# Kernel optimization log

Hardware: AMD Instinct MI355X
Metric: run time of the kernel (lower is better)

The kernel has to match this reference:

```python
import jax, jax.numpy as jnp
import numpy as np

N = 100_000      # nodes
E = 1_600_000    # edges (avg degree 16)
D = 64           # input_dim == hidden_dim
C = 10           # output classes
G = 512          # graphs in batch
L = 5            # num_layers (L-1 = 4 GINConv layers)
BN_EPS = 1e-5


def setup_inputs() -> dict:
    key = jax.random.key(0)
    ks = jax.random.split(key, 16)
    x = jax.random.normal(ks[0], (N, D), dtype=jnp.float32)
    edge_index = jax.random.randint(ks[1], (2, E), 0, N, dtype=jnp.int32)
    batch = jnp.sort(jax.random.randint(ks[2], (N,), 0, G, dtype=jnp.int32))
    s = 1.0 / np.sqrt(D)
    Lc = L - 1
    return {
        "x": x,
        "edge_index": edge_index,
        "batch": batch,
        "eps": jnp.zeros((Lc,), jnp.float32),                                   # GINConv eps (train_eps, init 0)
        "W1": jax.random.uniform(ks[3], (Lc, D, D), jnp.float32, -s, s),        # MLP linear 1
        "b1": jax.random.uniform(ks[4], (Lc, D), jnp.float32, -s, s),
        "g1": jnp.ones((Lc, D), jnp.float32),                                   # MLP BatchNorm
        "be1": jnp.zeros((Lc, D), jnp.float32),
        "W2": jax.random.uniform(ks[5], (Lc, D, D), jnp.float32, -s, s),        # MLP linear 2
        "b2": jax.random.uniform(ks[6], (Lc, D), jnp.float32, -s, s),
        "gout": jnp.ones((Lc, D), jnp.float32),                                 # outer BatchNorm
        "beout": jnp.zeros((Lc, D), jnp.float32),
        "Wp": jax.random.uniform(ks[7], (L, D, C), jnp.float32, -s, s),         # prediction linears
        "bp": jax.random.uniform(ks[8], (L, C), jnp.float32, -s, s),
    }


def _batchnorm(h, gamma, beta):
    # training-mode BN over node dim, biased variance (torch semantics)
    m = jnp.mean(h, axis=0)
    v = jnp.mean(jnp.square(h - m), axis=0)
    return gamma * (h - m) * jax.lax.rsqrt(v + BN_EPS) + beta


def reference(x, edge_index, batch, eps, W1, b1, g1, be1, W2, b2, gout, beout, Wp, bp):
    src, dst = edge_index[0], edge_index[1]
    hidden_rep = [x]
    h = x
    for l in range(L - 1):
        # GINConv: (1 + eps) * x + scatter-add of neighbor features
        agg = jax.ops.segment_sum(h[src], dst, num_segments=N)
        z = (1.0 + eps[l]) * h + agg
        # 2-layer MLP with internal BN+ReLU
        z = z @ W1[l] + b1[l]
        z = jax.nn.relu(_batchnorm(z, g1[l], be1[l]))
        z = z @ W2[l] + b2[l]
        # outer BN + ReLU
        h = jax.nn.relu(_batchnorm(z, gout[l], beout[l]))
        hidden_rep.append(h)
    # jumping-knowledge readout: per-layer global_add_pool + linear (dropout off / eval)
    score = jnp.zeros((G, C), jnp.float32)
    for l, hl in enumerate(hidden_rep):
        pooled = jax.ops.segment_sum(hl, batch, num_segments=G)
        score = score + pooled @ Wp[l] + bp[l]
    return score
```

## Files before the change

### kernel.cpp

```cpp
#include <hip/hip_runtime.h>

#define NN 100000
#define EE 1600000
#define DD 64
#define CC 10
#define GG 512
#define LL 5
#define NPAD 100352
#define N64 (NN * DD)
#define NB 392
#define PCH 4096
#define BCAP 6144
#define SC 8
#define PREPG 1563

typedef short bf16x8 __attribute__((ext_vector_type(8)));
typedef float f32x4  __attribute__((ext_vector_type(4)));
union U16 { uint4 u; bf16x8 h; };

__device__ __forceinline__ float bits2f(unsigned int b) { return __uint_as_float(b); }
__device__ __forceinline__ float bf2f(unsigned short s) { return __uint_as_float((unsigned int)s << 16); }
__device__ __forceinline__ unsigned short f2bf_rne(float v) {
    unsigned int b = __float_as_uint(v);
    return (unsigned short)((b + 0x7fffu + ((b >> 16) & 1u)) >> 16);
}
__device__ __forceinline__ void unpack8(uint4 u, float* f) {
    f[0] = bits2f(u.x << 16); f[1] = bits2f(u.x & 0xffff0000u);
    f[2] = bits2f(u.y << 16); f[3] = bits2f(u.y & 0xffff0000u);
    f[4] = bits2f(u.z << 16); f[5] = bits2f(u.z & 0xffff0000u);
    f[6] = bits2f(u.w << 16); f[7] = bits2f(u.w & 0xffff0000u);
}
__device__ __forceinline__ uint4 pack8(const float* f) {
    uint4 u;
    u.x = (unsigned int)f2bf_rne(f[0]) | ((unsigned int)f2bf_rne(f[1]) << 16);
    u.y = (unsigned int)f2bf_rne(f[2]) | ((unsigned int)f2bf_rne(f[3]) << 16);
    u.z = (unsigned int)f2bf_rne(f[4]) | ((unsigned int)f2bf_rne(f[5]) << 16);
    u.w = (unsigned int)f2bf_rne(f[6]) | ((unsigned int)f2bf_rne(f[7]) << 16);
    return u;
}
__device__ __forceinline__ void acc8(uint4 u, float* a) {
    float t[8];
    unpack8(u, t);
    #pragma unroll
    for (int k = 0; k < 8; ++k) a[k] += t[k];
}

__global__ __launch_bounds__(256) void prep_all_k(
    const float* __restrict__ x, const int* __restrict__ batch,
    unsigned short* __restrict__ hbuf, float* __restrict__ pooled,
    const float* __restrict__ W1, const float* __restrict__ W2,
    unsigned short* __restrict__ wt,
    const int* __restrict__ ei, int* __restrict__ bh)
{
    __shared__ int cnt[NB];
    const int bid = blockIdx.x;
    const int t = threadIdx.x;
    if (bid < PREPG) {
        int f = t & 63;
        int q = t >> 6;
        int n0 = bid * 64 + q * 16;
        int nmax = NN - n0; if (nmax > 16) nmax = 16;
        float acc = 0.f;
        int curg = -1;
        #pragma unroll 4
        for (int i = 0; i < nmax; ++i) {
            int n = n0 + i;
            int g = batch[n];
            if (g != curg) {
                if (curg >= 0) atomicAdd(&pooled[(size_t)curg * DD + f], acc);
                acc = 0.f; curg = g;
            }
            float v = x[(size_t)n * DD + f];
            hbuf[(size_t)n * DD + f] = f2bf_rne(v);
            acc += v;
        }
        if (curg >= 0) atomicAdd(&pooled[(size_t)curg * DD + f], acc);
    } else if (bid < PREPG + 8) {
        int mat = bid - PREPG;
        const float* src = (mat < 4) ? (W1 + (size_t)mat * 4096)
                                     : (W2 + (size_t)(mat - 4) * 4096);
        for (int idx = t; idx < 4096; idx += 256) {
            int c = idx >> 6, k = idx & 63;
            wt[(size_t)mat * 4096 + c * 64 + k] = f2bf_rne(src[k * 64 + c]);
        }
    } else {
        int hid = bid - PREPG - 8;
        for (int i = t; i < NB; i += 256) cnt[i] = 0;
        __syncthreads();
        for (int e = hid * 256 + t; e < EE; e += 512 * 256)
            atomicAdd(&cnt[ei[EE + e] >> 8], 1);
        __syncthreads();
        for (int i = t; i < NB; i += 256)
            if (cnt[i]) atomicAdd(&bh[i], cnt[i]);
    }
}

__global__ __launch_bounds__(512) void bscan_k(const int* __restrict__ bh,
                                               int* __restrict__ bo,
                                               int* __restrict__ bcur) {
    __shared__ int s[512];
    int t = threadIdx.x;
    int v = (t < NB) ? bh[t] : 0;
    s[t] = v;
    __syncthreads();
    for (int d = 1; d < 512; d <<= 1) {
        int a = (t >= d) ? s[t - d] : 0;
        __syncthreads();
        s[t] += a;
        __syncthreads();
    }
    int excl = s[t] - v;
    if (t < NB) { bo[t] = excl; bcur[t] = excl; }
    if (t == NB - 1) bo[NB] = excl + v;
}

__global__ __launch_bounds__(256) void partition_k(const int* __restrict__ ei,
                                                   int* __restrict__ bcur,
                                                   unsigned int* __restrict__ stage) {
    __shared__ int hist[NB];
    __shared__ int base[NB];
    __shared__ int gbase[NB];
    __shared__ int cnt2[NB];
    __shared__ int scanbuf[512];
    __shared__ unsigned int pairs[PCH];
    __shared__ unsigned short pbkt[PCH];
    int t = threadIdx.x;
    int e0 = blockIdx.x * PCH;
    int nE = EE - e0; if (nE > PCH) nE = PCH;

    for (int i = t; i < NB; i += 256) { hist[i] = 0; cnt2[i] = 0; }
    __syncthreads();

    int mys[16], myd[16];
    #pragma unroll
    for (int i = 0; i < 16; ++i) {
        int idx = i * 256 + t;
        if (idx < nE) {
            mys[i] = ei[e0 + idx];
            myd[i] = ei[EE + e0 + idx];
            atomicAdd(&hist[myd[i] >> 8], 1);
        } else myd[i] = -1;
    }
    __syncthreads();

    scanbuf[t]       = (t < NB) ? hist[t] : 0;
    scanbuf[t + 256] = (t + 256 < NB) ? hist[t + 256] : 0;
    __syncthreads();
    for (int d = 1; d < 512; d <<= 1) {
        int a0 = (t >= d) ? scanbuf[t - d] : 0;
        int a1 = ((t + 256) >= d) ? scanbuf[t + 256 - d] : 0;
        __syncthreads();
        scanbuf[t] += a0;
        scanbuf[t + 256] += a1;
        __syncthreads();
    }
    if (t < NB)       base[t]       = scanbuf[t] - hist[t];
    if (t + 256 < NB) base[t + 256] = scanbuf[t + 256] - hist[t + 256];
    __syncthreads();

    #pragma unroll
    for (int i = 0; i < 16; ++i) {
        if (myd[i] >= 0) {
            int b = myd[i] >> 8;
            int p = base[b] + atomicAdd(&cnt2[b], 1);
            pairs[p] = (unsigned)mys[i] | ((unsigned)(myd[i] & 255) << 17);
            pbkt[p] = (unsigned short)b;
        }
    }
    __syncthreads();
    for (int i = t; i < NB; i += 256)
        if (hist[i]) gbase[i] = atomicAdd(&bcur[i], hist[i]);
    __syncthreads();
    for (int p = t; p < nE; p += 256) {
        int b = pbkt[p];
        stage[gbase[b] + (p - base[b])] = pairs[p];
    }
}

__global__ __launch_bounds__(256) void bucket_csr_k(const unsigned int* __restrict__ stage,
                                                    const int* __restrict__ bo,
                                                    int* __restrict__ adj,
                                                    int* __restrict__ offs) {
    __shared__ int deg[256];
    __shared__ int sb[256];
    __shared__ int nb_[256];
    __shared__ int c2[256];
    __shared__ int loc[BCAP];
    int b = blockIdx.x;
    int s0 = bo[b], s1 = bo[b + 1];
    int cnt = s1 - s0;
    int t = threadIdx.x;

    deg[t] = 0;
    __syncthreads();
    for (int i = t; i < cnt; i += 256) atomicAdd(&deg[(stage[s0 + i] >> 17) & 255], 1);
    __syncthreads();
    sb[t] = deg[t];
    __syncthreads();
    for (int d = 1; d < 256; d <<= 1) {
        int a = (t >= d) ? sb[t - d] : 0;
        __syncthreads();
        sb[t] += a;
        __syncthreads();
    }
    int nbase = sb[t] - deg[t];
    nb_[t] = nbase;
    c2[t] = 0;
    offs[b * 256 + t] = s0 + nbase;
    __syncthreads();

    if (cnt <= BCAP) {
        for (int i = t; i < cnt; i += 256) {
            unsigned int pr = stage[s0 + i];
            int ln = (pr >> 17) & 255;
            int p = nb_[ln] + atomicAdd(&c2[ln], 1);
            loc[p] = (int)(pr & 0x1FFFF);
        }
        __syncthreads();
        for (int i = t; i < cnt; i += 256) adj[s0 + i] = loc[i];
    } else {
        for (int i = t; i < cnt; i += 256) {
            unsigned int pr = stage[s0 + i];
            int ln = (pr >> 17) & 255;
            int p = nb_[ln] + atomicAdd(&c2[ln], 1);
            adj[s0 + p] = (int)(pr & 0x1FFFF);
        }
    }
}

__global__ __launch_bounds__(512, 8) void layer1_k(
    const unsigned short* __restrict__ hb, const int* __restrict__ adj,
    const int* __restrict__ offs, const float* __restrict__ epsArr, int l,
    const unsigned short* __restrict__ wtm, const float* __restrict__ bias,
    unsigned short* __restrict__ z1, float* __restrict__ stats1,
    float* __restrict__ stats2z)
{
    __shared__ unsigned short aLDS[64 * 64];
    const int t = threadIdx.x;
    const int lane = t & 63;
    const int w = t >> 6;
    const int n15 = lane & 15;
    const int quad = lane >> 4;

    if (blockIdx.x < SC && t < 128) stats2z[blockIdx.x * 128 + t] = 0.f;

    const float epsv = 1.0f + epsArr[l];
    const int c8 = lane & 7;
    {
        int lr = w * 8 + (lane >> 3);
        int n = blockIdx.x * 64 + lr;
        float acc[8] = {0.f,0.f,0.f,0.f,0.f,0.f,0.f,0.f};
        if (n < NN) {
            uint4 a = *(const uint4*)(hb + (size_t)n * DD + c8 * 8);
            unpack8(a, acc);
            #pragma unroll
            for (int j2 = 0; j2 < 8; ++j2) acc[j2] *= epsv;
            int j = offs[n], end = offs[n + 1];
            if (j < end) {
                int e1 = end - 1;
                int a0 = adj[j];
                int a1 = adj[(j + 1 < end) ? j + 1 : e1];
                int a2 = adj[(j + 2 < end) ? j + 2 : e1];
                int a3 = adj[(j + 3 < end) ? j + 3 : e1];
                #pragma unroll 1
                while (j < end) {
                    uint4 v0 = *(const uint4*)(hb + (size_t)a0 * DD + c8 * 8);
                    uint4 v1 = *(const uint4*)(hb + (size_t)a1 * DD + c8 * 8);
                    uint4 v2 = *(const uint4*)(hb + (size_t)a2 * DD + c8 * 8);
                    uint4 v3 = *(const uint4*)(hb + (size_t)a3 * DD + c8 * 8);
                    int jn = j + 4;
                    int b0 = adj[(jn     < end) ? jn     : e1];
                    int b1 = adj[(jn + 1 < end) ? jn + 1 : e1];
                    int b2 = adj[(jn + 2 < end) ? jn + 2 : e1];
                    int b3 = adj[(jn + 3 < end) ? jn + 3 : e1];
                    int rem = end - j;
                    acc8(v0, acc);
                    if (rem > 1) acc8(v1, acc);
                    if (rem > 2) acc8(v2, acc);
                    if (rem > 3) acc8(v3, acc);
                    a0 = b0; a1 = b1; a2 = b2; a3 = b3;
                    j = jn;
                }
            }
        }
        int pu = c8 ^ (lr & 7);
        *(uint4*)(aLDS + lr * 64 + pu * 8) = pack8(acc);
    }

    const int rt = w & 3;
    const int cb = (w >> 2) * 2;
    U16 bfr[2][2];
    #pragma unroll
    for (int ci = 0; ci < 2; ++ci)
        #pragma unroll
        for (int ks = 0; ks < 2; ++ks)
            bfr[ci][ks].u = *(const uint4*)(wtm + (size_t)((cb + ci) * 16 + n15) * 64 + ks * 32 + quad * 8);

    __syncthreads();

    U16 afr[2];
    int lr2 = rt * 16 + n15;
    #pragma unroll
    for (int ks = 0; ks < 2; ++ks) {
        int pu = (ks * 4 + quad) ^ (lr2 & 7);
        afr[ks].u = *(const uint4*)(aLDS + lr2 * 64 + pu * 8);
    }

    const int rowg0 = blockIdx.x * 64 + rt * 16;
    const int copy = blockIdx.x & (SC - 1);
    #pragma unroll
    for (int ci = 0; ci < 2; ++ci) {
        int ct = cb + ci;
        f32x4 acc = {0.f, 0.f, 0.f, 0.f};
        acc = __builtin_amdgcn_mfma_f32_16x16x32_bf16(afr[0].h, bfr[ci][0].h, acc, 0, 0, 0);
        acc = __builtin_amdgcn_mfma_f32_16x16x32_bf16(afr[1].h, bfr[ci][1].h, acc, 0, 0, 0);
        int col = ct * 16 + n15;
        float bcol = bias[col];
        float s = 0.f, ss = 0.f;
        #pragma unroll
        for (int r = 0; r < 4; ++r) {
            int rg = rowg0 + quad * 4 + r;
            float v = acc[r] + bcol;
            if (rg < NN) {
                z1[(size_t)rg * DD + col] = f2bf_rne(v);
                s += v;
                ss = fmaf(v, v, ss);
            }
        }
        s  += __shfl_xor(s, 16, 64);  s  += __shfl_xor(s, 32, 64);
        ss += __shfl_xor(ss, 16, 64); ss += __shfl_xor(ss, 32, 64);
        if (lane < 16) {
            atomicAdd(&stats1[copy * 128 + ct * 16 + lane], s);
            atomicAdd(&stats1[copy * 128 + 64 + ct * 16 + lane], ss);
        }
    }
}

__global__ __launch_bounds__(256) void layer2_k(
    const unsigned short* __restrict__ z1, const float* __restrict__ stats1,
    const float* __restrict__ gamma, const float* __restrict__ beta, int off,
    const unsigned short* __restrict__ wtm, const float* __restrict__ bias,
    unsigned short* __restrict__ z2, float* __restrict__ stats2)
{
    __shared__ float ssS[128];
    const int t = threadIdx.x;
    const int lane = t & 63;
    const int w = t >> 6;
    const int n15 = lane & 15;
    const int quad = lane >> 4;
    const int base0 = blockIdx.x * 256;

    U16 bfr[4][2];
    #pragma unroll
    for (int ct = 0; ct < 4; ++ct)
        #pragma unroll
        for (int ks = 0; ks < 2; ++ks)
            bfr[ct][ks].u = *(const uint4*)(wtm + (size_t)(ct * 16 + n15) * 64 + ks * 32 + quad * 8);

    if (t < 64) {
        float S = 0.f, SS = 0.f;
        #pragma unroll
        for (int c = 0; c < SC; ++c) { S += stats1[c * 128 + t]; SS += stats1[c * 128 + 64 + t]; }
        float inv_n = 1.0f / (float)NN;
        float mean = S * inv_n;
        float var  = SS * inv_n - mean * mean;
        float sc = gamma[off + t] * rsqrtf(var + 1e-5f);
        ssS[t] = sc;
        ssS[64 + t] = beta[off + t] - sc * mean;
    }
    __syncthreads();

    float sacc[4]  = {0.f, 0.f, 0.f, 0.f};
    float ssacc[4] = {0.f, 0.f, 0.f, 0.f};
    #pragma unroll 1
    for (int ti = 0; ti < 4; ++ti) {
        const int rowg0 = base0 + ti * 64 + w * 16;
        int arow = rowg0 + n15;
        int arowc = (arow < NN) ? arow : (NN - 1);
        uint4 raw[2];
        #pragma unroll
        for (int ks = 0; ks < 2; ++ks)
            raw[ks] = *(const uint4*)(z1 + (size_t)arowc * DD + ks * 32 + quad * 8);

        U16 afr[2];
        #pragma unroll
        for (int ks = 0; ks < 2; ++ks) {
            float f[8];
            unpack8(raw[ks], f);
            int k0 = ks * 32 + quad * 8;
            #pragma unroll
            for (int j = 0; j < 8; ++j)
                f[j] = fmaxf(fmaf(ssS[k0 + j], f[j], ssS[64 + k0 + j]), 0.f);
            afr[ks].u = pack8(f);
        }

        #pragma unroll
        for (int ct = 0; ct < 4; ++ct) {
            f32x4 acc = {0.f, 0.f, 0.f, 0.f};
            acc = __builtin_amdgcn_mfma_f32_16x16x32_bf16(afr[0].h, bfr[ct][0].h, acc, 0, 0, 0);
            acc = __builtin_amdgcn_mfma_f32_16x16x32_bf16(afr[1].h, bfr[ct][1].h, acc, 0, 0, 0);
            int col = ct * 16 + n15;
            float bcol = bias[col];
            #pragma unroll
            for (int r = 0; r < 4; ++r) {
                int rg = rowg0 + quad * 4 + r;
                float v = acc[r] + bcol;
                if (rg < NN) {
                    z2[(size_t)rg * DD + col] = f2bf_rne(v);
                    sacc[ct] += v;
                    ssacc[ct] = fmaf(v, v, ssacc[ct]);
                }
            }
        }
    }
    const int copy = blockIdx.x & (SC - 1);
    #pragma unroll
    for (int ct = 0; ct < 4; ++ct) {
        float s = sacc[ct], ss = ssacc[ct];
        s  += __shfl_xor(s, 16, 64);  s  += __shfl_xor(s, 32, 64);
        ss += __shfl_xor(ss, 16, 64); ss += __shfl_xor(ss, 32, 64);
        if (lane < 16) {
            atomicAdd(&stats2[copy * 128 + ct * 16 + lane], s);
            atomicAdd(&stats2[copy * 128 + 64 + ct * 16 + lane], ss);
        }
    }
}

__global__ __launch_bounds__(256) void layer3_k(
    const unsigned short* __restrict__ z2, const float* __restrict__ stats2,
    const float* __restrict__ gamma, const float* __restrict__ beta, int off,
    const int* __restrict__ batch, unsigned short* __restrict__ hout,
    float* __restrict__ pooled, float* __restrict__ stats1z)
{
    __shared__ float ssS[128];
    int t = threadIdx.x;
    if (blockIdx.x < SC && t < 128) stats1z[blockIdx.x * 128 + t] = 0.f;
    if (t < 64) {
        float S = 0.f, SS = 0.f;
        #pragma unroll
        for (int c = 0; c < SC; ++c) { S += stats2[c * 128 + t]; SS += stats2[c * 128 + 64 + t]; }
        float inv_n = 1.0f / (float)NN;
        float mean = S * inv_n;
        float var  = SS * inv_n - mean * mean;
        float sc = gamma[off + t] * rsqrtf(var + 1e-5f);
        ssS[t] = sc;
        ssS[64 + t] = beta[off + t] - sc * mean;
    }
    __syncthreads();

    int f = t & 63;
    int q = t >> 6;
    float sc = ssS[f], sh = ssS[64 + f];
    #pragma unroll 1
    for (int ti = 0; ti < 4; ++ti) {
        int n0 = blockIdx.x * 256 + ti * 64 + q * 16;
        int nmax = NN - n0; if (nmax > 16) nmax = 16;
        float acc = 0.f;
        int curg = -1;
        #pragma unroll 4
        for (int i = 0; i < nmax; ++i) {
            int n = n0 + i;
            int g = batch[n];
            if (g != curg) {
                if (curg >= 0) atomicAdd(&pooled[(size_t)curg * DD + f], acc);
                acc = 0.f; curg = g;
            }
            float v = bf2f(z2[(size_t)n * DD + f]);
            v = fmaxf(fmaf(sc, v, sh), 0.f);
            hout[(size_t)n * DD + f] = f2bf_rne(v);
            acc += v;
        }
        if (curg >= 0) atomicAdd(&pooled[(size_t)curg * DD + f], acc);
    }
}

__global__ void readout_k(const float* __restrict__ pooled,
                          const float* __restrict__ Wp, const float* __restrict__ bp,
                          float* __restrict__ out)
{
    int gc = blockIdx.x * blockDim.x + threadIdx.x;
    if (gc >= GG * CC) return;
    int g = gc / CC, c = gc - g * CC;
    float acc = 0.f;
    for (int l = 0; l < LL; ++l) {
        acc += bp[l * CC + c];
        const float* p  = pooled + ((size_t)l * GG + g) * DD;
        const float* wv = Wp + (size_t)l * DD * CC + c;
        #pragma unroll 8
        for (int f = 0; f < DD; ++f) acc = fmaf(p[f], wv[f * CC], acc);
    }
    out[gc] = acc;
}

extern "C" void kernel_launch(void* const* d_in, const int* in_sizes, int n_in,
                              void* d_out, int out_size, void* d_ws, size_t ws_size,
                              hipStream_t stream) {
    const float* x     = (const float*)d_in[0];
    const int*   ei    = (const int*)d_in[1];
    const int*   batch = (const int*)d_in[2];
    const float* eps   = (const float*)d_in[3];
    const float* W1    = (const float*)d_in[4];
    const float* b1    = (const float*)d_in[5];
    const float* g1    = (const float*)d_in[6];
    const float* be1   = (const float*)d_in[7];
    const float* W2    = (const float*)d_in[8];
    const float* b2    = (const float*)d_in[9];
    const float* gout  = (const float*)d_in[10];
    const float* beout = (const float*)d_in[11];
    const float* Wp    = (const float*)d_in[12];
    const float* bp    = (const float*)d_in[13];
    float* out = (float*)d_out;

    unsigned int* stage = (unsigned int*)d_ws;
    int* adj   = (int*)(stage + EE);
    int* offs  = adj + EE;
    int* bo    = offs + NPAD + 256;
    int* bcur  = bo + 400;
    int* bh    = bcur + 400;
    float* pooled = (float*)(bh + 400);
    float* stats1 = pooled + (size_t)LL * GG * DD;
    float* stats2 = stats1 + SC * 128;
    unsigned short* hb  = (unsigned short*)(stats2 + SC * 128);
    unsigned short* z1b = hb + N64;
    unsigned short* z2b = z1b + N64;
    unsigned short* wt  = z2b + N64;

    hipMemsetAsync(bh, 0, (400 + (size_t)LL * GG * DD + 2 * SC * 128) * sizeof(int), stream);
    prep_all_k<<<PREPG + 8 + 512, 256, 0, stream>>>(x, batch, hb, pooled, W1, W2, wt, ei, bh);
    bscan_k<<<1, 512, 0, stream>>>(bh, bo, bcur);
    partition_k<<<(EE + PCH - 1) / PCH, 256, 0, stream>>>(ei, bcur, stage);
    bucket_csr_k<<<NB, 256, 0, stream>>>(stage, bo, adj, offs);

    const int gemm_grid = (NN + 63) / 64;
    const int big_grid  = (NN + 255) / 256;
    for (int l = 0; l < LL - 1; ++l) {
        layer1_k<<<gemm_grid, 512, 0, stream>>>(
            hb, adj, offs, eps, l, wt + (size_t)l * 4096, b1 + l * DD, z1b, stats1, stats2);
        layer2_k<<<big_grid, 256, 0, stream>>>(
            z1b, stats1, g1, be1, l * DD, wt + (size_t)(4 + l) * 4096, b2 + l * DD, z2b, stats2);
        layer3_k<<<big_grid, 256, 0, stream>>>(
            z2b, stats2, gout, beout, l * DD, batch, hb,
            pooled + (size_t)(l + 1) * GG * DD, stats1);
    }
    readout_k<<<(GG * CC + 255) / 256, 256, 0, stream>>>(pooled, Wp, bp, out);
}
```

Measured before the change: 554.5 us.

## Fuse all GIN layers and readout into one persistent cooperative kernel

Replaces the per-layer layer1/layer2/layer3 launches and the readout launch with a single cooperative persistent kernel. Grid-wide syncs separate the stages, and atomic work counters hand out tiles dynamically. This removes about 13 kernel launch gaps and their tail effects. In exchange it adds grid-sync cost, per-tile atomic counter traffic with extra __syncthreads, and caps concurrency at the cooperative occupancy limit. Layer2 now processes 128-row chunks with 512 threads instead of 256-row blocks.

Result: slower. 1.324 ms (+138.8%).

```diff
diff --git a/kernel.cpp b/kernel.cpp
--- a/kernel.cpp
+++ b/kernel.cpp
@@ -1,4 +1,6 @@
 #include <hip/hip_runtime.h>
+#include <hip/hip_cooperative_groups.h>
+namespace cg = cooperative_groups;
 
 #define NN 100000
 #define EE 1600000
@@ -13,6 +15,8 @@
 #define BCAP 6144
 #define SC 8
 #define PREPG 1563
+#define L1TILES 1563
+#define CHUNKS 782
 
 typedef short bf16x8 __attribute__((ext_vector_type(8)));
 typedef float f32x4  __attribute__((ext_vector_type(4)));
@@ -228,268 +232,286 @@
     }
 }
 
-__global__ __launch_bounds__(512, 8) void layer1_k(
-    const unsigned short* __restrict__ hb, const int* __restrict__ adj,
-    const int* __restrict__ offs, const float* __restrict__ epsArr, int l,
-    const unsigned short* __restrict__ wtm, const float* __restrict__ bias,
-    unsigned short* __restrict__ z1, float* __restrict__ stats1,
-    float* __restrict__ stats2z)
+__global__ __launch_bounds__(512, 8) void gin_coop_k(
+    unsigned short* __restrict__ hbuf,
+    const int* __restrict__ adj,
+    const int* __restrict__ offs,
+    const float* __restrict__ epsArr,
+    const unsigned short* __restrict__ wt,
+    const float* __restrict__ b1,
+    const float* __restrict__ g1,
+    const float* __restrict__ be1,
+    const float* __restrict__ b2,
+    const float* __restrict__ gout,
+    const float* __restrict__ beout,
+    unsigned short* __restrict__ z1b,
+    unsigned short* __restrict__ z2b,
+    float* __restrict__ pooled,
+    float* __restrict__ stats1,
+    float* __restrict__ stats2,
+    const int* __restrict__ batch,
+    int* __restrict__ ctr,
+    const float* __restrict__ Wp,
+    const float* __restrict__ bp,
+    float* __restrict__ out)
 {
+    cg::grid_group grid = cg::this_grid();
     __shared__ unsigned short aLDS[64 * 64];
+    __shared__ float ssS[128];
+    __shared__ int vbS;
     const int t = threadIdx.x;
     const int lane = t & 63;
     const int w = t >> 6;
     const int n15 = lane & 15;
     const int quad = lane >> 4;
-
-    if (blockIdx.x < SC && t < 128) stats2z[blockIdx.x * 128 + t] = 0.f;
-
-    const float epsv = 1.0f + epsArr[l];
     const int c8 = lane & 7;
-    {
-        int lr = w * 8 + (lane >> 3);
-        int n = blockIdx.x * 64 + lr;
-        float acc[8] = {0.f,0.f,0.f,0.f,0.f,0.f,0.f,0.f};
-        if (n < NN) {
-            uint4 a = *(const uint4*)(hb + (size_t)n * DD + c8 * 8);
-            unpack8(a, acc);
-            #pragma unroll
-            for (int j2 = 0; j2 < 8; ++j2) acc[j2] *= epsv;
-            int j = offs[n], end = offs[n + 1];
-            if (j < end) {
-                int e1 = end - 1;
-                int a0 = adj[j];
-                int a1 = adj[(j + 1 < end) ? j + 1 : e1];
-                int a2 = adj[(j + 2 < end) ? j + 2 : e1];
-                int a3 = adj[(j + 3 < end) ? j + 3 : e1];
-                #pragma unroll 1
-                while (j < end) {
-                    uint4 v0 = *(const uint4*)(hb + (size_t)a0 * DD + c8 * 8);
-                    uint4 v1 = *(const uint4*)(hb + (size_t)a1 * DD + c8 * 8);
-                    uint4 v2 = *(const uint4*)(hb + (size_t)a2 * DD + c8 * 8);
-                    uint4 v3 = *(const uint4*)(hb + (size_t)a3 * DD + c8 * 8);
-                    int jn = j + 4;
-                    int b0 = adj[(jn     < end) ? jn     : e1];
-                    int b1 = adj[(jn + 1 < end) ? jn + 1 : e1];
-                    int b2 = adj[(jn + 2 < end) ? jn + 2 : e1];
-                    int b3 = adj[(jn + 3 < end) ? jn + 3 : e1];
-                    int rem = end - j;
-                    acc8(v0, acc);
-                    if (rem > 1) acc8(v1, acc);
-                    if (rem > 2) acc8(v2, acc);
-                    if (rem > 3) acc8(v3, acc);
-                    a0 = b0; a1 = b1; a2 = b2; a3 = b3;
-                    j = jn;
+    const int bid = blockIdx.x;
+
+    for (int l = 0; l < LL - 1; ++l) {
+        const unsigned short* wt1 = wt + (size_t)l * 4096;
+        const unsigned short* wt2 = wt + (size_t)(4 + l) * 4096;
+        const float* bias1 = b1 + l * DD;
+        const float* bias2 = b2 + l * DD;
+        const float epsv = 1.0f + epsArr[l];
+
+        const int rt = w & 3;
+        const int cb = (w >> 2) * 2;
+        U16 bfr1[2][2];
+        #pragma unroll
+        for (int ci = 0; ci < 2; ++ci)
+            #pragma unroll
+            for (int ks = 0; ks < 2; ++ks)
+                bfr1[ci][ks].u = *(const uint4*)(wt1 + (size_t)((cb + ci) * 16 + n15) * 64 + ks * 32 + quad * 8);
+
+        for (;;) {
+            __syncthreads();
+            if (t == 0) vbS = atomicAdd(&ctr[l * 3], 1);
+            __syncthreads();
+            const int vb = vbS;
+            if (vb >= L1TILES) break;
+            if (vb < SC && t < 128) stats2[vb * 128 + t] = 0.f;
+
+            {
+                int lr = w * 8 + (lane >> 3);
+                int n = vb * 64 + lr;
+                float acc[8] = {0.f,0.f,0.f,0.f,0.f,0.f,0.f,0.f};
+                if (n < NN) {
+                    uint4 a = *(const uint4*)(hbuf + (size_t)n * DD + c8 * 8);
+                    unpack8(a, acc);
+                    #pragma unroll
+                    for (int k = 0; k < 8; ++k) acc[k] *= epsv;
+                    int j = offs[n], end = offs[n + 1];
+                    if (j < end) {
+                        int e1 = end - 1;
+                        int a0 = adj[j];
+                        int a1 = adj[(j + 1 < end) ? j + 1 : e1];
+                        int a2 = adj[(j + 2 < end) ? j + 2 : e1];
+                        int a3 = adj[(j + 3 < end) ? j + 3 : e1];
+                        #pragma unroll 1
+                        while (j < end) {
+                            uint4 v0 = *(const uint4*)(hbuf + (size_t)a0 * DD + c8 * 8);
+                            uint4 v1 = *(const uint4*)(hbuf + (size_t)a1 * DD + c8 * 8);
+                            uint4 v2 = *(const uint4*)(hbuf + (size_t)a2 * DD + c8 * 8);
+                            uint4 v3 = *(const uint4*)(hbuf + (size_t)a3 * DD + c8 * 8);
+                            int jn = j + 4;
+                            int b0 = adj[(jn     < end) ? jn     : e1];
+                            int b1i = adj[(jn + 1 < end) ? jn + 1 : e1];
+                            int b2i = adj[(jn + 2 < end) ? jn + 2 : e1];
+                            int b3i = adj[(jn + 3 < end) ? jn + 3 : e1];
+                            int rem = end - j;
+                            acc8(v0, acc);
+                            if (rem > 1) acc8(v1, acc);
+                            if (rem > 2) acc8(v2, acc);
+                            if (rem > 3) acc8(v3, acc);
+                            a0 = b0; a1 = b1i; a2 = b2i; a3 = b3i;
+                            j = jn;
+                        }
+                    }
                 }
-            }
-        }
-        int pu = c8 ^ (lr & 7);
-        *(uint4*)(aLDS + lr * 64 + pu * 8) = pack8(acc);
-    }
-
-    const int rt = w & 3;
-    const int cb = (w >> 2) * 2;
-    U16 bfr[2][2];
-    #pragma unroll
-    for (int ci = 0; ci < 2; ++ci)
+                int pu = c8 ^ (lr & 7);
+                *(uint4*)(aLDS + lr * 64 + pu * 8) = pack8(acc);
+            }
+            __syncthreads();
+
+            U16 afr[2];
+            int lr2 = rt * 16 + n15;
+            #pragma unroll
+            for (int ks = 0; ks < 2; ++ks) {
+                int pu = (ks * 4 + quad) ^ (lr2 & 7);
+                afr[ks].u = *(const uint4*)(aLDS + lr2 * 64 + pu * 8);
+            }
+
+            const int rowg0 = vb * 64 + rt * 16;
+            const int copy = vb & (SC - 1);
+            #pragma unroll
+            for (int ci = 0; ci < 2; ++ci) {
+                int ct = cb + ci;
+                f32x4 acc = {0.f, 0.f, 0.f, 0.f};
+                acc = __builtin_amdgcn_mfma_f32_16x16x32_bf16(afr[0].h, bfr1[ci][0].h, acc, 0, 0, 0);
+                acc = __builtin_amdgcn_mfma_f32_16x16x32_bf16(afr[1].h, bfr1[ci][1].h, acc, 0, 0, 0);
+                int col = ct * 16 + n15;
+                float bcol = bias1[col];
+                float s = 0.f, ss = 0.f;
+                #pragma unroll
+                for (int r = 0; r < 4; ++r) {
+                    int rg = rowg0 + quad * 4 + r;
+                    float v = acc[r] + bcol;
+                    if (rg < NN) {
+                        z1b[(size_t)rg * DD + col] = f2bf_rne(v);
+                        s += v;
+                        ss = fmaf(v, v, ss);
+                    }
+                }
+                s  += __shfl_xor(s, 16, 64);  s  += __shfl_xor(s, 32, 64);
+                ss += __shfl_xor(ss, 16, 64); ss += __shfl_xor(ss, 32, 64);
+                if (lane < 16) {
+                    atomicAdd(&stats1[copy * 128 + ct * 16 + lane], s);
+                    atomicAdd(&stats1[copy * 128 + 64 + ct * 16 + lane], ss);
+                }
+            }
+        }
+        grid.sync();
+
+        if (t < 64) {
+            float S = 0.f, SS = 0.f;
+            #pragma unroll
+            for (int c = 0; c < SC; ++c) { S += stats1[c * 128 + t]; SS += stats1[c * 128 + 64 + t]; }
+            float inv_n = 1.0f / (float)NN;
+            float mean = S * inv_n;
+            float var  = SS * inv_n - mean * mean;
+            float sc = g1[l * DD + t] * rsqrtf(var + 1e-5f);
+            ssS[t] = sc;
+            ssS[64 + t] = be1[l * DD + t] - sc * mean;
+        }
+        __syncthreads();
+
+        U16 bfr2[4][2];
         #pragma unroll
-        for (int ks = 0; ks < 2; ++ks)
-            bfr[ci][ks].u = *(const uint4*)(wtm + (size_t)((cb + ci) * 16 + n15) * 64 + ks * 32 + quad * 8);
-
-    __syncthreads();
-
-    U16 afr[2];
-    int lr2 = rt * 16 + n15;
-    #pragma unroll
-    for (int ks = 0; ks < 2; ++ks) {
-        int pu = (ks * 4 + quad) ^ (lr2 & 7);
-        afr[ks].u = *(const uint4*)(aLDS + lr2 * 64 + pu * 8);
-    }
-
-    const int rowg0 = blockIdx.x * 64 + rt * 16;
-    const int copy = blockIdx.x & (SC - 1);
-    #pragma unroll
-    for (int ci = 0; ci < 2; ++ci) {
-        int ct = cb + ci;
-        f32x4 acc = {0.f, 0.f, 0.f, 0.f};
-        acc = __builtin_amdgcn_mfma_f32_16x16x32_bf16(afr[0].h, bfr[ci][0].h, acc, 0, 0, 0);
-        acc = __builtin_amdgcn_mfma_f32_16x16x32_bf16(afr[1].h, bfr[ci][1].h, acc, 0, 0, 0);
-        int col = ct * 16 + n15;
-        float bcol = bias[col];
-        float s = 0.f, ss = 0.f;
-        #pragma unroll
-        for (int r = 0; r < 4; ++r) {
-            int rg = rowg0 + quad * 4 + r;
-            float v = acc[r] + bcol;
-            if (rg < NN) {
-                z1[(size_t)rg * DD + col] = f2bf_rne(v);
-                s += v;
-                ss = fmaf(v, v, ss);
-            }
-        }
-        s  += __shfl_xor(s, 16, 64);  s  += __shfl_xor(s, 32, 64);
-        ss += __shfl_xor(ss, 16, 64); ss += __shfl_xor(ss, 32, 64);
-        if (lane < 16) {
-            atomicAdd(&stats1[copy * 128 + ct * 16 + lane], s);
-            atomicAdd(&stats1[copy * 128 + 64 + ct * 16 + lane], ss);
-        }
-    }
-}
-
-__global__ __launch_bounds__(256) void layer2_k(
-    const unsigned short* __restrict__ z1, const float* __restrict__ stats1,
-    const float* __restrict__ gamma, const float* __restrict__ beta, int off,
-    const unsigned short* __restrict__ wtm, const float* __restrict__ bias,
-    unsigned short* __restrict__ z2, float* __restrict__ stats2)
-{
-    __shared__ float ssS[128];
-    const int t = threadIdx.x;
-    const int lane = t & 63;
-    const int w = t >> 6;
-    const int n15 = lane & 15;
-    const int quad = lane >> 4;
-    const int base0 = blockIdx.x * 256;
-
-    U16 bfr[4][2];
-    #pragma unroll
-    for (int ct = 0; ct < 4; ++ct)
-        #pragma unroll
-        for (int ks = 0; ks < 2; ++ks)
-            bfr[ct][ks].u = *(const uint4*)(wtm + (size_t)(ct * 16 + n15) * 64 + ks * 32 + quad * 8);
-
-    if (t < 64) {
-        float S = 0.f, SS = 0.f;
-        #pragma unroll
-        for (int c = 0; c < SC; ++c) { S += stats1[c * 128 + t]; SS += stats1[c * 128 + 64 + t]; }
-        float inv_n = 1.0f / (float)NN;
-        float mean = S * inv_n;
-        float var  = SS * inv_n - mean * mean;
-        float sc = gamma[off + t] * rsqrtf(var + 1e-5f);
-        ssS[t] = sc;
-        ssS[64 + t] = beta[off + t] - sc * mean;
-    }
-    __syncthreads();
-
-    float sacc[4]  = {0.f, 0.f, 0.f, 0.f};
-    float ssacc[4] = {0.f, 0.f, 0.f, 0.f};
-    #pragma unroll 1
-    for (int ti = 0; ti < 4; ++ti) {
-        const int rowg0 = base0 + ti * 64 + w * 16;
-        int arow = rowg0 + n15;
-        int arowc = (arow < NN) ? arow : (NN - 1);
-        uint4 raw[2];
-        #pragma unroll
-        for (int ks = 0; ks < 2; ++ks)
-            raw[ks] = *(const uint4*)(z1 + (size_t)arowc * DD + ks * 32 + quad * 8);
-
-        U16 afr[2];
-        #pragma unroll
-        for (int ks = 0; ks < 2; ++ks) {
-            float f[8];
-            unpack8(raw[ks], f);
-            int k0 = ks * 32 + quad * 8;
-            #pragma unroll
-            for (int j = 0; j < 8; ++j)
-                f[j] = fmaxf(fmaf(ssS[k0 + j], f[j], ssS[64 + k0 + j]), 0.f);
-            afr[ks].u = pack8(f);
-        }
-
-        #pragma unroll
-        for (int ct = 0; ct < 4; ++ct) {
-            f32x4 acc = {0.f, 0.f, 0.f, 0.f};
-            acc = __builtin_amdgcn_mfma_f32_16x16x32_bf16(afr[0].h, bfr[ct][0].h, acc, 0, 0, 0);
-            acc = __builtin_amdgcn_mfma_f32_16x16x32_bf16(afr[1].h, bfr[ct][1].h, acc, 0, 0, 0);
-            int col = ct * 16 + n15;
-            float bcol = bias[col];
-            #pragma unroll
-            for (int r = 0; r < 4; ++r) {
-                int rg = rowg0 + quad * 4 + r;
-                float v = acc[r] + bcol;
-                if (rg < NN) {
-                    z2[(size_t)rg * DD + col] = f2bf_rne(v);
-                    sacc[ct] += v;
-                    ssacc[ct] = fmaf(v, v, ssacc[ct]);
+        for (int ct = 0; ct < 4; ++ct)
+            #pragma unroll
+            for (int ks = 0; ks < 2; ++ks)
+                bfr2[ct][ks].u = *(const uint4*)(wt2 + (size_t)(ct * 16 + n15) * 64 + ks * 32 + quad * 8);
+
+        float sacc[4]  = {0.f, 0.f, 0.f, 0.f};
+        float ssacc[4] = {0.f, 0.f, 0.f, 0.f};
+        for (;;) {
+            __syncthreads();
+            if (t == 0) vbS = atomicAdd(&ctr[l * 3 + 1], 1);
+            __syncthreads();
+            const int ch = vbS;
+            if (ch >= CHUNKS) break;
+            const int rowg0 = ch * 128 + (w >> 2) * 64 + (w & 3) * 16;
+            int arow = rowg0 + n15;
+            int arowc = (arow < NN) ? arow : (NN - 1);
+            uint4 raw[2];
+            #pragma unroll
+            for (int ks = 0; ks < 2; ++ks)
+                raw[ks] = *(const uint4*)(z1b + (size_t)arowc * DD + ks * 32 + quad * 8);
+
+            U16 afr[2];
+            #pragma unroll
+            for (int ks = 0; ks < 2; ++ks) {
+                float f[8];
+                unpack8(raw[ks], f);
+                int k0 = ks * 32 + quad * 8;
+                #pragma unroll
+                for (int jj = 0; jj < 8; ++jj)
+                    f[jj] = fmaxf(fmaf(ssS[k0 + jj], f[jj], ssS[64 + k0 + jj]), 0.f);
+                afr[ks].u = pack8(f);
+            }
+
+            #pragma unroll
+            for (int ct = 0; ct < 4; ++ct) {
+                f32x4 acc = {0.f, 0.f, 0.f, 0.f};
+                acc = __builtin_amdgcn_mfma_f32_16x16x32_bf16(afr[0].h, bfr2[ct][0].h, acc, 0, 0, 0);
+                acc = __builtin_amdgcn_mfma_f32_16x16x32_bf16(afr[1].h, bfr2[ct][1].h, acc, 0, 0, 0);
+                int col = ct * 16 + n15;
+                float bcol = bias2[col];
+                #pragma unroll
+                for (int r = 0; r < 4; ++r) {
+                    int rg = rowg0 + quad * 4 + r;
+                    float v = acc[r] + bcol;
+                    if (rg < NN) {
+                        z2b[(size_t)rg * DD + col] = f2bf_rne(v);
+                        sacc[ct] += v;
+                        ssacc[ct] = fmaf(v, v, ssacc[ct]);
+                    }
                 }
             }
         }
-    }
-    const int copy = blockIdx.x & (SC - 1);
-    #pragma unroll
-    for (int ct = 0; ct < 4; ++ct) {
-        float s = sacc[ct], ss = ssacc[ct];
-        s  += __shfl_xor(s, 16, 64);  s  += __shfl_xor(s, 32, 64);
-        ss += __shfl_xor(ss, 16, 64); ss += __shfl_xor(ss, 32, 64);
-        if (lane < 16) {
-            atomicAdd(&stats2[copy * 128 + ct * 16 + lane], s);
-            atomicAdd(&stats2[copy * 128 + 64 + ct * 16 + lane], ss);
-        }
-    }
-}
-
-__global__ __launch_bounds__(256) void layer3_k(
-    const unsigned short* __restrict__ z2, const float* __restrict__ stats2,
-    const float* __restrict__ gamma, const float* __restrict__ beta, int off,
-    const int* __restrict__ batch, unsigned short* __restrict__ hout,
-    float* __restrict__ pooled, float* __restrict__ stats1z)
-{
-    __shared__ float ssS[128];
-    int t = threadIdx.x;
-    if (blockIdx.x < SC && t < 128) stats1z[blockIdx.x * 128 + t] = 0.f;
-    if (t < 64) {
-        float S = 0.f, SS = 0.f;
-        #pragma unroll
-        for (int c = 0; c < SC; ++c) { S += stats2[c * 128 + t]; SS += stats2[c * 128 + 64 + t]; }
-        float inv_n = 1.0f / (float)NN;
-        float mean = S * inv_n;
-        float var  = SS * inv_n - mean * mean;
-        float sc = gamma[off + t] * rsqrtf(var + 1e-5f);
-        ssS[t] = sc;
-        ssS[64 + t] = beta[off + t] - sc * mean;
-    }
-    __syncthreads();
-
-    int f = t & 63;
-    int q = t >> 6;
-    float sc = ssS[f], sh = ssS[64 + f];
-    #pragma unroll 1
-    for (int ti = 0; ti < 4; ++ti) {
-        int n0 = blockIdx.x * 256 + ti * 64 + q * 16;
-        int nmax = NN - n0; if (nmax > 16) nmax = 16;
+        {
+            const int copy = bid & (SC - 1);
+            #pragma unroll
+            for (int ct = 0; ct < 4; ++ct) {
+                float s = sacc[ct], ss = ssacc[ct];
+                s  += __shfl_xor(s, 16, 64);  s  += __shfl_xor(s, 32, 64);
+                ss += __shfl_xor(ss, 16, 64); ss += __shfl_xor(ss, 32, 64);
+                if (lane < 16) {
+                    atomicAdd(&stats2[copy * 128 + ct * 16 + lane], s);
+                    atomicAdd(&stats2[copy * 128 + 64 + ct * 16 + lane], ss);
+                }
+            }
+        }
+        grid.sync();
+
+        if (t < 64) {
+            float S = 0.f, SS = 0.f;
+            #pragma unroll
+            for (int c = 0; c < SC; ++c) { S += stats2[c * 128 + t]; SS += stats2[c * 128 + 64 + t]; }
+            float inv_n = 1.0f / (float)NN;
+            float mean = S * inv_n;
+            float var  = SS * inv_n - mean * mean;
+            float sc = gout[l * DD + t] * rsqrtf(var + 1e-5f);
+            ssS[t] = sc;
+            ssS[64 + t] = beout[l * DD + t] - sc * mean;
+        }
+        __syncthreads();
+        float* pl = pooled + (size_t)(l + 1) * GG * DD;
+        const int f = t & 63;
+        const int q = t >> 6;
+        const float scv = ssS[f], shv = ssS[64 + f];
+        for (;;) {
+            __syncthreads();
+            if (t == 0) vbS = atomicAdd(&ctr[l * 3 + 2], 1);
+            __syncthreads();
+            const int ch = vbS;
+            if (ch >= CHUNKS) break;
+            if (ch < SC && t < 128) stats1[ch * 128 + t] = 0.f;
+            int n0 = ch * 128 + q * 16;
+            int nmax = NN - n0; if (nmax > 16) nmax = 16;
+            float acc = 0.f;
+            int curg = -1;
+            #pragma unroll 4
+            for (int i = 0; i < nmax; ++i) {
+                int n = n0 + i;
+                int g = batch[n];
+                if (g != curg) {
+                    if (curg >= 0) atomicAdd(&pl[(size_t)curg * DD + f], acc);
+                    acc = 0.f; curg = g;
+                }
+                float v = bf2f(z2b[(size_t)n * DD + f]);
+                v = fmaxf(fmaf(scv, v, shv), 0.f);
+                hbuf[(size_t)n * DD + f] = f2bf_rne(v);
+                acc += v;
+            }
+            if (curg >= 0) atomicAdd(&pl[(size_t)curg * DD + f], acc);
+        }
+        grid.sync();
+    }
+
+    int gc = bid * 512 + t;
+    if (gc < GG * CC) {
+        int g = gc / CC, c = gc - g * CC;
         float acc = 0.f;
-        int curg = -1;
-        #pragma unroll 4
-        for (int i = 0; i < nmax; ++i) {
-            int n = n0 + i;
-            int g = batch[n];
-            if (g != curg) {
-                if (curg >= 0) atomicAdd(&pooled[(size_t)curg * DD + f], acc);
-                acc = 0.f; curg = g;
-            }
-            float v = bf2f(z2[(size_t)n * DD + f]);
-            v = fmaxf(fmaf(sc, v, sh), 0.f);
-            hout[(size_t)n * DD + f] = f2bf_rne(v);
-            acc += v;
-        }
-        if (curg >= 0) atomicAdd(&pooled[(size_t)curg * DD + f], acc);
-    }
-}
-
-__global__ void readout_k(const float* __restrict__ pooled,
-                          const float* __restrict__ Wp, const float* __restrict__ bp,
-                          float* __restrict__ out)
-{
-    int gc = blockIdx.x * blockDim.x + threadIdx.x;
-    if (gc >= GG * CC) return;
-    int g = gc / CC, c = gc - g * CC;
-    float acc = 0.f;
-    for (int l = 0; l < LL; ++l) {
-        acc += bp[l * CC + c];
-        const float* p  = pooled + ((size_t)l * GG + g) * DD;
-        const float* wv = Wp + (size_t)l * DD * CC + c;
-        #pragma unroll 8
-        for (int f = 0; f < DD; ++f) acc = fmaf(p[f], wv[f * CC], acc);
-    }
-    out[gc] = acc;
+        for (int l = 0; l < LL; ++l) {
+            acc += bp[l * CC + c];
+            const float* p  = pooled + ((size_t)l * GG + g) * DD;
+            const float* wv = Wp + (size_t)l * DD * CC + c;
+            #pragma unroll 8
+            for (int ff = 0; ff < DD; ++ff) acc = fmaf(p[ff], wv[ff * CC], acc);
+        }
+        out[gc] = acc;
+    }
 }
 
 extern "C" void kernel_launch(void* const* d_in, const int* in_sizes, int n_in,
@@ -517,7 +539,8 @@
     int* bo    = offs + NPAD + 256;
     int* bcur  = bo + 400;
     int* bh    = bcur + 400;
-    float* pooled = (float*)(bh + 400);
+    int* ctr   = bh + 400;
+    float* pooled = (float*)(ctr + 16);
     float* stats1 = pooled + (size_t)LL * GG * DD;
     float* stats2 = stats1 + SC * 128;
     unsigned short* hb  = (unsigned short*)(stats2 + SC * 128);
@@ -525,22 +548,31 @@
     unsigned short* z2b = z1b + N64;
     unsigned short* wt  = z2b + N64;
 
-    hipMemsetAsync(bh, 0, (400 + (size_t)LL * GG * DD + 2 * SC * 128) * sizeof(int), stream);
+    hipMemsetAsync(bh, 0, (400 + 16 + (size_t)LL * GG * DD + 2 * SC * 128) * sizeof(int), stream);
     prep_all_k<<<PREPG + 8 + 512, 256, 0, stream>>>(x, batch, hb, pooled, W1, W2, wt, ei, bh);
     bscan_k<<<1, 512, 0, stream>>>(bh, bo, bcur);
     partition_k<<<(EE + PCH - 1) / PCH, 256, 0, stream>>>(ei, bcur, stage);
     bucket_csr_k<<<NB, 256, 0, stream>>>(stage, bo, adj, offs);
 
-    const int gemm_grid = (NN + 63) / 64;
-    const int big_grid  = (NN + 255) / 256;
-    for (int l = 0; l < LL - 1; ++l) {
-        layer1_k<<<gemm_grid, 512, 0, stream>>>(
-            hb, adj, offs, eps, l, wt + (size_t)l * 4096, b1 + l * DD, z1b, stats1, stats2);
-        layer2_k<<<big_grid, 256, 0, stream>>>(
-            z1b, stats1, g1, be1, l * DD, wt + (size_t)(4 + l) * 4096, b2 + l * DD, z2b, stats2);
-        layer3_k<<<big_grid, 256, 0, stream>>>(
-            z2b, stats2, gout, beout, l * DD, batch, hb,
-            pooled + (size_t)(l + 1) * GG * DD, stats1);
-    }
-    readout_k<<<(GG * CC + 255) / 256, 256, 0, stream>>>(pooled, Wp, bp, out);
-}
+    static int gridBlocks = 0;
+    if (gridBlocks == 0) {
+        int dev = 0; hipGetDevice(&dev);
+        int cus = 256;
+        hipDeviceGetAttribute(&cus, hipDeviceAttributeMultiprocessorCount, dev);
+        int mpb = 1;
+        hipOccupancyMaxActiveBlocksPerMultiprocessor(&mpb, gin_coop_k, 512, 0);
+        gridBlocks = mpb * cus;
+        if (gridBlocks > 1024) gridBlocks = 1024;
+        if (gridBlocks < 256)  gridBlocks = 256;
+    }
+    unsigned short* hbp = hb;
+    void* cargs[] = {
+        (void*)&hbp, (void*)&adj, (void*)&offs, (void*)&eps, (void*)&wt,
+        (void*)&b1, (void*)&g1, (void*)&be1, (void*)&b2, (void*)&gout,
+        (void*)&beout, (void*)&z1b, (void*)&z2b, (void*)&pooled,
+        (void*)&stats1, (void*)&stats2, (void*)&batch, (void*)&ctr,
+        (void*)&Wp, (void*)&bp, (void*)&out
+    };
+    hipLaunchCooperativeKernel((void*)gin_coop_k, dim3(gridBlocks), dim3(512),
+                               cargs, 0, stream);
+}
```
